# Optimization experiments

Hardware: AMD Instinct MI355X
Metric: run time of the kernel (lower is better)

The kernel has to match this reference:

```python
import jax, jax.numpy as jnp
import numpy as np

N_EMBD = 1024
HEAD_SIZE = 64


def setup_inputs() -> dict:
    key = jax.random.key(0)
    kx, kq, kk, kv = jax.random.split(key, 4)
    B, T = 8, 2048
    x = jax.random.normal(kx, (B, T, N_EMBD), dtype=jnp.float32)
    s = 1.0 / np.sqrt(N_EMBD)
    Wq = jax.random.normal(kq, (N_EMBD, HEAD_SIZE), dtype=jnp.float32) * s
    Wk = jax.random.normal(kk, (N_EMBD, HEAD_SIZE), dtype=jnp.float32) * s
    Wv = jax.random.normal(kv, (N_EMBD, HEAD_SIZE), dtype=jnp.float32) * s
    return {"x": x, "Wq": Wq, "Wk": Wk, "Wv": Wv}


def reference(x, Wq, Wk, Wv):
    # x: [B, T, C]; W*: [C, H]
    q = jnp.einsum('btc,ch->bth', x, Wq)
    k = jnp.einsum('btc,ch->bth', x, Wk)
    v = jnp.einsum('btc,ch->bth', x, Wv)
    H = q.shape[-1]
    score = jnp.einsum('bth,bsh->bts', q, k) / jnp.sqrt(jnp.asarray(H, q.dtype))
    T = score.shape[-1]
    causal = jnp.tril(jnp.ones((T, T), dtype=bool))  # [T, T]
    score = jnp.where(causal, score, -jnp.inf)
    attn = jax.nn.softmax(score, axis=-1)
    return jnp.einsum('bts,bsh->bth', attn, v)
```

## Files before the change

kernel.cpp:

```cpp
#include <hip/hip_runtime.h>

typedef __bf16 bf16;
typedef __attribute__((ext_vector_type(8))) __bf16 bf16x8;
typedef __attribute__((ext_vector_type(4))) __bf16 bf16x4;
typedef __attribute__((ext_vector_type(4))) float floatx4;

#define MFMA16(a, b, c) __builtin_amdgcn_mfma_f32_16x16x32_bf16((a), (b), (c), 0, 0, 0)

__global__ void prep_w(const float* __restrict__ Wq, const float* __restrict__ Wk,
                       const float* __restrict__ Wv, bf16* __restrict__ wTf) {
    int tid = blockIdx.x * 256 + threadIdx.x;
    int j = tid & 7;
    int l = (tid >> 3) & 15;
    int q = (tid >> 7) & 3;
    int kc = (tid >> 9) & 31;
    int mt = tid >> 14;
    int mat = mt >> 2;
    int h = ((mt & 3) << 4) + l;
    int c = kc * 32 + q * 8 + j;
    const float* W = (mat == 0) ? Wq : (mat == 1) ? Wk : Wv;
    wTf[tid] = (bf16)W[c * 64 + h];
}

#define XSTR 1032

__global__ __launch_bounds__(256, 4) void proj_qkv(const float* __restrict__ x,
                                                   const bf16* __restrict__ wTf,
                                                   bf16* __restrict__ q,
                                                   bf16* __restrict__ k,
                                                   bf16* __restrict__ vT) {
    __shared__ bf16 xs[16 * XSTR];

    const int tid = threadIdx.x;
    const int lane = tid & 63;
    const int w = tid >> 6;
    const int l15 = lane & 15;
    const int quad = lane >> 4;
    const int T0 = blockIdx.x * 16;

    {
        const int r = tid >> 4;
        const int cm = tid & 15;
        const float* g = x + (size_t)(T0 + r) * 1024 + cm * 8;
        floatx4 f[16];
        #pragma unroll
        for (int c = 0; c < 8; c++) {
            f[2 * c]     = *(const floatx4*)(g + c * 128);
            f[2 * c + 1] = *(const floatx4*)(g + c * 128 + 4);
        }
        bf16* ld = xs + r * XSTR + cm * 8;
        #pragma unroll
        for (int c = 0; c < 8; c++) {
            bf16x8 pk;
            pk[0] = (bf16)f[2*c][0]; pk[1] = (bf16)f[2*c][1];
            pk[2] = (bf16)f[2*c][2]; pk[3] = (bf16)f[2*c][3];
            pk[4] = (bf16)f[2*c+1][0]; pk[5] = (bf16)f[2*c+1][1];
            pk[6] = (bf16)f[2*c+1][2]; pk[7] = (bf16)f[2*c+1][3];
            *(bf16x8*)(ld + c * 128) = pk;
        }
    }
    __syncthreads();

    floatx4 acc[3] = {};
    const bf16* aw0 = wTf + (size_t)(w * 3 + 0) * 16384 + lane * 8;
    const bf16* aw1 = wTf + (size_t)(w * 3 + 1) * 16384 + lane * 8;
    const bf16* aw2 = wTf + (size_t)(w * 3 + 2) * 16384 + lane * 8;
    const bf16* xr = xs + l15 * XSTR + quad * 8;

    bf16x8 a0c = *(const bf16x8*)(aw0);
    bf16x8 a1c = *(const bf16x8*)(aw1);
    bf16x8 a2c = *(const bf16x8*)(aw2);
    bf16x8 a0n = *(const bf16x8*)(aw0 + 512);
    bf16x8 a1n = *(const bf16x8*)(aw1 + 512);
    bf16x8 a2n = *(const bf16x8*)(aw2 + 512);

    #pragma unroll 4
    for (int kc = 0; kc < 32; kc++) {
        bf16x8 p0 = *(const bf16x8*)(aw0 + (kc + 2) * 512);
        bf16x8 p1 = *(const bf16x8*)(aw1 + (kc + 2) * 512);
        bf16x8 p2 = *(const bf16x8*)(aw2 + (kc + 2) * 512);
        bf16x8 bb = *(const bf16x8*)(xr + kc * 32);
        acc[0] = MFMA16(a0c, bb, acc[0]);
        acc[1] = MFMA16(a1c, bb, acc[1]);
        acc[2] = MFMA16(a2c, bb, acc[2]);
        a0c = a0n; a1c = a1n; a2c = a2n;
        a0n = p0;  a1n = p1;  a2n = p2;
    }

    const int t = T0 + l15;
    #pragma unroll
    for (int i = 0; i < 3; i++) {
        int mtile = w * 3 + i;
        int mat = mtile >> 2;
        int hbase = ((mtile & 3) << 4) + (quad << 2);
        float sc = (mat == 0) ? 0.125f : 1.0f;
        bf16x4 pk;
        pk[0] = (bf16)(acc[i][0] * sc);
        pk[1] = (bf16)(acc[i][1] * sc);
        pk[2] = (bf16)(acc[i][2] * sc);
        pk[3] = (bf16)(acc[i][3] * sc);
        if (mat == 0) {
            *(bf16x4*)(q + (size_t)t * 64 + hbase) = pk;
        } else if (mat == 1) {
            *(bf16x4*)(k + (size_t)t * 64 + hbase) = pk;
        } else {
            int b = t >> 11, tt = t & 2047;
            #pragma unroll
            for (int r = 0; r < 4; r++)
                vT[(size_t)(b * 64 + hbase + r) * 2048 + tt] = pk[r];
        }
    }
}

#define KP2 72
#define OH 68

__global__ __launch_bounds__(512, 4) void flash(const bf16* __restrict__ q,
                                                const bf16* __restrict__ k,
                                                const bf16* __restrict__ vT,
                                                float* __restrict__ out) {
    __shared__ char smem[8 * 16 * OH * 4];
    __shared__ float Ms[8][16], Ls[8][16];
    bf16* psall = (bf16*)smem;
    float* Os = (float*)smem;

    const int b = blockIdx.x & 7;
    const int p = blockIdx.x >> 3;
    const int t0A = p * 16;
    const int t0B = (127 - p) * 16;
    const int nttA = (p >> 2) + 1;
    const int nttB = ((127 - p) >> 2) + 1;
    const int L = nttA + nttB;

    const int tid = threadIdx.x;
    const int w = tid >> 6;
    const int lane = tid & 63;
    const int l15 = lane & 15;
    const int quad = lane >> 4;

    const int s0 = (L * w) >> 3;
    const int s1 = (L * (w + 1)) >> 3;

    const bf16* kbase = k + (size_t)(b * 2048 + l15) * 64 + quad * 8;
    const bf16* vbase = vT + (size_t)(b * 64 + l15) * 2048 + quad * 8;
    bf16* psw = psall + w * 16 * KP2;

    const bf16* qpA = q + (size_t)(b * 2048 + t0A + l15) * 64 + quad * 8;
    const bf16* qpB = q + (size_t)(b * 2048 + t0B + l15) * 64 + quad * 8;

    floatx4 oA[4] = {}, oB[4] = {};
    float miA = -1e30f, liA = 0.f, miB = -1e30f, liB = 0.f;

#define KV_STEP(jtv, isdiag, t0v, qf0v, qf1v, mi_, li_, o_)                          \
    {                                                                                 \
        const bf16* kp = kbase + (size_t)(jtv) * 4096;                                \
        floatx4 stt[4];                                                               \
        _Pragma("unroll") for (int mt = 0; mt < 4; mt++) {                            \
            floatx4 z = {};                                                           \
            bf16x8 ka0 = *(const bf16x8*)(kp + mt * 1024);                            \
            bf16x8 ka1 = *(const bf16x8*)(kp + mt * 1024 + 32);                       \
            z = MFMA16(ka0, qf0v, z);                                                 \
            z = MFMA16(ka1, qf1v, z);                                                 \
            stt[mt] = z;                                                              \
        }                                                                             \
        if (isdiag) {                                                                 \
            _Pragma("unroll") for (int mt = 0; mt < 4; mt++)                          \
                _Pragma("unroll") for (int r = 0; r < 4; r++) {                       \
                    int kv = (jtv) * 64 + mt * 16 + quad * 4 + r;                     \
                    if (kv > (t0v) + l15) stt[mt][r] = -1e30f;                        \
                }                                                                     \
        }                                                                             \
        float mx = fmaxf(fmaxf(fmaxf(stt[0][0], stt[0][1]), fmaxf(stt[0][2], stt[0][3])),  \
                         fmaxf(fmaxf(stt[1][0], stt[1][1]), fmaxf(stt[1][2], stt[1][3]))); \
        mx = fmaxf(mx, fmaxf(fmaxf(fmaxf(stt[2][0], stt[2][1]), fmaxf(stt[2][2], stt[2][3])),  \
                             fmaxf(fmaxf(stt[3][0], stt[3][1]), fmaxf(stt[3][2], stt[3][3])))); \
        mx = fmaxf(mx, __shfl_xor(mx, 16, 64));                                       \
        mx = fmaxf(mx, __shfl_xor(mx, 32, 64));                                       \
        float mnew = fmaxf(mi_, mx);                                                  \
        float aa = __expf(mi_ - mnew);                                                \
        mi_ = mnew;                                                                   \
        float rs = 0.f;                                                               \
        _Pragma("unroll") for (int mt = 0; mt < 4; mt++)                              \
            _Pragma("unroll") for (int r = 0; r < 4; r++) {                           \
                float pv = __expf(stt[mt][r] - mnew);                                 \
                stt[mt][r] = pv;                                                      \
                rs += pv;                                                             \
            }                                                                         \
        rs += __shfl_xor(rs, 16, 64);                                                 \
        rs += __shfl_xor(rs, 32, 64);                                                 \
        li_ = li_ * aa + rs;                                                          \
        _Pragma("unroll") for (int mt = 0; mt < 4; mt++)                              \
            _Pragma("unroll") for (int r = 0; r < 4; r++) o_[mt][r] *= aa;            \
        _Pragma("unroll") for (int mt = 0; mt < 4; mt++) {                            \
            bf16x4 pk;                                                                \
            pk[0] = (bf16)stt[mt][0]; pk[1] = (bf16)stt[mt][1];                       \
            pk[2] = (bf16)stt[mt][2]; pk[3] = (bf16)stt[mt][3];                       \
            *(bf16x4*)(psw + l15 * KP2 + mt * 16 + quad * 4) = pk;                    \
        }                                                                             \
        const bf16* vp = vbase + (jtv) * 64;                                          \
        _Pragma("unroll") for (int kc = 0; kc < 2; kc++) {                            \
            bf16x8 pb = *(const bf16x8*)(psw + l15 * KP2 + kc * 32 + quad * 8);       \
            _Pragma("unroll") for (int mt = 0; mt < 4; mt++) {                        \
                bf16x8 va = *(const bf16x8*)(vp + mt * 32768 + kc * 32);              \
                o_[mt] = MFMA16(va, pb, o_[mt]);                                      \
            }                                                                         \
        }                                                                             \
    }

    {
        const int eA = (s1 < nttA) ? s1 : nttA;
        if (s0 < eA) {
            bf16x8 qf0 = *(const bf16x8*)qpA;
            bf16x8 qf1 = *(const bf16x8*)(qpA + 32);
            for (int s = s0; s < eA; s++) {
                KV_STEP(s, (s == nttA - 1), t0A, qf0, qf1, miA, liA, oA);
            }
        }
    }
    {
        const int sB = (s0 > nttA) ? s0 : nttA;
        if (sB < s1) {
            bf16x8 qf0 = *(const bf16x8*)qpB;
            bf16x8 qf1 = *(const bf16x8*)(qpB + 32);
            for (int s = sB; s < s1; s++) {
                KV_STEP(s - nttA, (s == L - 1), t0B, qf0, qf1, miB, liB, oB);
            }
        }
    }

    #pragma unroll
    for (int tile = 0; tile < 2; tile++) {
        __syncthreads();
        float mi = tile ? miB : miA;
        float li = tile ? liB : liA;
        if (lane < 16) { Ms[w][lane] = mi; Ls[w][lane] = li; }
        #pragma unroll
        for (int mt = 0; mt < 4; mt++) {
            floatx4 ov = tile ? oB[mt] : oA[mt];
            *(floatx4*)(Os + (w * 16 + l15) * OH + mt * 16 + quad * 4) = ov;
        }
        __syncthreads();
        {
            int qq = tid >> 5;
            int h2 = (tid & 31) * 2;
            float Mg = -1e30f;
            #pragma unroll
            for (int u = 0; u < 8; u++) Mg = fmaxf(Mg, Ms[u][qq]);
            float Lg = 0.f, v0 = 0.f, v1 = 0.f;
            #pragma unroll
            for (int u = 0; u < 8; u++) {
                float sw = __expf(Ms[u][qq] - Mg);
                Lg += sw * Ls[u][qq];
                const float* Or = Os + (u * 16 + qq) * OH + h2;
                v0 += sw * Or[0];
                v1 += sw * Or[1];
            }
            float inv = 1.0f / Lg;
            int t0v = tile ? t0B : t0A;
            float* op = out + (size_t)(b * 2048 + t0v + qq) * 64 + h2;
            op[0] = v0 * inv;
            op[1] = v1 * inv;
        }
    }
#undef KV_STEP
}

extern "C" void kernel_launch(void* const* d_in, const int* in_sizes, int n_in,
                              void* d_out, int out_size, void* d_ws, size_t ws_size,
                              hipStream_t stream) {
    const float* x  = (const float*)d_in[0];
    const float* Wq = (const float*)d_in[1];
    const float* Wk = (const float*)d_in[2];
    const float* Wv = (const float*)d_in[3];
    float* out = (float*)d_out;

    char* ws = (char*)d_ws;
    bf16* wTf = (bf16*)ws;
    bf16* q   = (bf16*)(ws + 397312);
    bf16* k   = (bf16*)(ws + 397312 + 2097152);
    bf16* vT  = (bf16*)(ws + 397312 + 2 * 2097152);

    hipLaunchKernelGGL(prep_w,   dim3(768),  dim3(256), 0, stream, Wq, Wk, Wv, wTf);
    hipLaunchKernelGGL(proj_qkv, dim3(1024), dim3(256), 0, stream, x, wTf, q, k, vT);
    hipLaunchKernelGGL(flash,    dim3(512),  dim3(512), 0, stream, q, k, vT, out);
}
```

Before: 144.1 us.

## Double projection row tile, swizzle LDS, and add lazy rescale with exp2 softmax

The projection kernel now handles 32 rows per block instead of 16, so each weight fragment loaded from global memory feeds two MFMAs. The x tile in shared memory uses an XOR swizzle in place of padding, and the grid is halved with launch bounds lowered to 2. In the flash kernel, Q is pre-scaled by log2(e)/8 so the softmax can use native exp2. The running-max rescale is skipped when the new max exceeds the old one by at most 8 (in log2 units), and s_setprio raises wave priority around the MFMA blocks. These changes cut weight-load traffic, exponential cost and rescale work, at the price of a larger LDS footprint per block, lower occupancy, and bounded growth of the unnormalized values.

Result: faster. 140.0 us (-2.9%).

```diff
diff --git a/kernel.cpp b/kernel.cpp
--- a/kernel.cpp
+++ b/kernel.cpp
@@ -22,50 +22,55 @@
     wTf[tid] = (bf16)W[c * 64 + h];
 }
 
-#define XSTR 1032
-
-__global__ __launch_bounds__(256, 4) void proj_qkv(const float* __restrict__ x,
+__global__ __launch_bounds__(256, 2) void proj_qkv(const float* __restrict__ x,
                                                    const bf16* __restrict__ wTf,
                                                    bf16* __restrict__ q,
                                                    bf16* __restrict__ k,
                                                    bf16* __restrict__ vT) {
-    __shared__ bf16 xs[16 * XSTR];
+    __shared__ __align__(16) char xsb[32 * 2048];
 
     const int tid = threadIdx.x;
     const int lane = tid & 63;
     const int w = tid >> 6;
     const int l15 = lane & 15;
     const int quad = lane >> 4;
-    const int T0 = blockIdx.x * 16;
+    const int T0 = blockIdx.x * 32;
 
     {
         const int r = tid >> 4;
         const int cm = tid & 15;
-        const float* g = x + (size_t)(T0 + r) * 1024 + cm * 8;
-        floatx4 f[16];
         #pragma unroll
-        for (int c = 0; c < 8; c++) {
-            f[2 * c]     = *(const floatx4*)(g + c * 128);
-            f[2 * c + 1] = *(const floatx4*)(g + c * 128 + 4);
-        }
-        bf16* ld = xs + r * XSTR + cm * 8;
-        #pragma unroll
-        for (int c = 0; c < 8; c++) {
-            bf16x8 pk;
-            pk[0] = (bf16)f[2*c][0]; pk[1] = (bf16)f[2*c][1];
-            pk[2] = (bf16)f[2*c][2]; pk[3] = (bf16)f[2*c][3];
-            pk[4] = (bf16)f[2*c+1][0]; pk[5] = (bf16)f[2*c+1][1];
-            pk[6] = (bf16)f[2*c+1][2]; pk[7] = (bf16)f[2*c+1][3];
-            *(bf16x8*)(ld + c * 128) = pk;
+        for (int half = 0; half < 2; half++) {
+            const int row = r + half * 16;
+            const float* g = x + (size_t)(T0 + row) * 1024 + cm * 8;
+            floatx4 f[16];
+            #pragma unroll
+            for (int c = 0; c < 8; c++) {
+                f[2 * c]     = *(const floatx4*)(g + c * 128);
+                f[2 * c + 1] = *(const floatx4*)(g + c * 128 + 4);
+            }
+            char* ldb = xsb + row * 2048;
+            const int sxs = (row & 7) << 4;
+            #pragma unroll
+            for (int c = 0; c < 8; c++) {
+                bf16x8 pk;
+                pk[0] = (bf16)f[2*c][0]; pk[1] = (bf16)f[2*c][1];
+                pk[2] = (bf16)f[2*c][2]; pk[3] = (bf16)f[2*c][3];
+                pk[4] = (bf16)f[2*c+1][0]; pk[5] = (bf16)f[2*c+1][1];
+                pk[6] = (bf16)f[2*c+1][2]; pk[7] = (bf16)f[2*c+1][3];
+                *(bf16x8*)(ldb + ((cm * 16 + c * 256) ^ sxs)) = pk;
+            }
         }
     }
     __syncthreads();
 
-    floatx4 acc[3] = {};
+    floatx4 acc[6] = {};
     const bf16* aw0 = wTf + (size_t)(w * 3 + 0) * 16384 + lane * 8;
     const bf16* aw1 = wTf + (size_t)(w * 3 + 1) * 16384 + lane * 8;
     const bf16* aw2 = wTf + (size_t)(w * 3 + 2) * 16384 + lane * 8;
-    const bf16* xr = xs + l15 * XSTR + quad * 8;
+    const char* xr = xsb + l15 * 2048;
+    const int sx = (l15 & 7) << 4;
+    const int q16 = quad * 16;
 
     bf16x8 a0c = *(const bf16x8*)(aw0);
     bf16x8 a1c = *(const bf16x8*)(aw1);
@@ -79,35 +84,44 @@
         bf16x8 p0 = *(const bf16x8*)(aw0 + (kc + 2) * 512);
         bf16x8 p1 = *(const bf16x8*)(aw1 + (kc + 2) * 512);
         bf16x8 p2 = *(const bf16x8*)(aw2 + (kc + 2) * 512);
-        bf16x8 bb = *(const bf16x8*)(xr + kc * 32);
-        acc[0] = MFMA16(a0c, bb, acc[0]);
-        acc[1] = MFMA16(a1c, bb, acc[1]);
-        acc[2] = MFMA16(a2c, bb, acc[2]);
+        const int o = (kc * 64 + q16) ^ sx;
+        bf16x8 b0 = *(const bf16x8*)(xr + o);
+        bf16x8 b1 = *(const bf16x8*)(xr + 32768 + o);
+        acc[0] = MFMA16(a0c, b0, acc[0]);
+        acc[1] = MFMA16(a0c, b1, acc[1]);
+        acc[2] = MFMA16(a1c, b0, acc[2]);
+        acc[3] = MFMA16(a1c, b1, acc[3]);
+        acc[4] = MFMA16(a2c, b0, acc[4]);
+        acc[5] = MFMA16(a2c, b1, acc[5]);
         a0c = a0n; a1c = a1n; a2c = a2n;
         a0n = p0;  a1n = p1;  a2n = p2;
     }
 
-    const int t = T0 + l15;
     #pragma unroll
     for (int i = 0; i < 3; i++) {
         int mtile = w * 3 + i;
         int mat = mtile >> 2;
         int hbase = ((mtile & 3) << 4) + (quad << 2);
-        float sc = (mat == 0) ? 0.125f : 1.0f;
-        bf16x4 pk;
-        pk[0] = (bf16)(acc[i][0] * sc);
-        pk[1] = (bf16)(acc[i][1] * sc);
-        pk[2] = (bf16)(acc[i][2] * sc);
-        pk[3] = (bf16)(acc[i][3] * sc);
-        if (mat == 0) {
-            *(bf16x4*)(q + (size_t)t * 64 + hbase) = pk;
-        } else if (mat == 1) {
-            *(bf16x4*)(k + (size_t)t * 64 + hbase) = pk;
-        } else {
-            int b = t >> 11, tt = t & 2047;
-            #pragma unroll
-            for (int r = 0; r < 4; r++)
-                vT[(size_t)(b * 64 + hbase + r) * 2048 + tt] = pk[r];
+        float sc = (mat == 0) ? 0.18033688011112042f : 1.0f;
+        #pragma unroll
+        for (int tt = 0; tt < 2; tt++) {
+            const int t = T0 + tt * 16 + l15;
+            floatx4 av = acc[i * 2 + tt];
+            bf16x4 pk;
+            pk[0] = (bf16)(av[0] * sc);
+            pk[1] = (bf16)(av[1] * sc);
+            pk[2] = (bf16)(av[2] * sc);
+            pk[3] = (bf16)(av[3] * sc);
+            if (mat == 0) {
+                *(bf16x4*)(q + (size_t)t * 64 + hbase) = pk;
+            } else if (mat == 1) {
+                *(bf16x4*)(k + (size_t)t * 64 + hbase) = pk;
+            } else {
+                int bidx = t >> 11, tmod = t & 2047;
+                #pragma unroll
+                for (int r = 0; r < 4; r++)
+                    vT[(size_t)(bidx * 64 + hbase + r) * 2048 + tmod] = pk[r];
+            }
         }
     }
 }
@@ -155,6 +169,7 @@
     {                                                                                 \
         const bf16* kp = kbase + (size_t)(jtv) * 4096;                                \
         floatx4 stt[4];                                                               \
+        __builtin_amdgcn_s_setprio(1);                                                \
         _Pragma("unroll") for (int mt = 0; mt < 4; mt++) {                            \
             floatx4 z = {};                                                           \
             bf16x8 ka0 = *(const bf16x8*)(kp + mt * 1024);                            \
@@ -163,6 +178,7 @@
             z = MFMA16(ka1, qf1v, z);                                                 \
             stt[mt] = z;                                                              \
         }                                                                             \
+        __builtin_amdgcn_s_setprio(0);                                                \
         if (isdiag) {                                                                 \
             _Pragma("unroll") for (int mt = 0; mt < 4; mt++)                          \
                 _Pragma("unroll") for (int r = 0; r < 4; r++) {                       \
@@ -176,21 +192,25 @@
                              fmaxf(fmaxf(stt[3][0], stt[3][1]), fmaxf(stt[3][2], stt[3][3])))); \
         mx = fmaxf(mx, __shfl_xor(mx, 16, 64));                                       \
         mx = fmaxf(mx, __shfl_xor(mx, 32, 64));                                       \
-        float mnew = fmaxf(mi_, mx);                                                  \
-        float aa = __expf(mi_ - mnew);                                                \
-        mi_ = mnew;                                                                   \
+        const bool nodefer = !__all(mx - mi_ <= 8.0f);                                \
+        const float mnew = nodefer ? fmaxf(mi_, mx) : mi_;                            \
         float rs = 0.f;                                                               \
         _Pragma("unroll") for (int mt = 0; mt < 4; mt++)                              \
             _Pragma("unroll") for (int r = 0; r < 4; r++) {                           \
-                float pv = __expf(stt[mt][r] - mnew);                                 \
+                float pv = __builtin_amdgcn_exp2f(stt[mt][r] - mnew);                 \
                 stt[mt][r] = pv;                                                      \
                 rs += pv;                                                             \
             }                                                                         \
         rs += __shfl_xor(rs, 16, 64);                                                 \
         rs += __shfl_xor(rs, 32, 64);                                                 \
-        li_ = li_ * aa + rs;                                                          \
-        _Pragma("unroll") for (int mt = 0; mt < 4; mt++)                              \
-            _Pragma("unroll") for (int r = 0; r < 4; r++) o_[mt][r] *= aa;            \
+        if (nodefer) {                                                                \
+            const float aa = __builtin_amdgcn_exp2f(mi_ - mnew);                      \
+            mi_ = mnew;                                                               \
+            li_ *= aa;                                                                \
+            _Pragma("unroll") for (int mt = 0; mt < 4; mt++)                          \
+                _Pragma("unroll") for (int r = 0; r < 4; r++) o_[mt][r] *= aa;        \
+        }                                                                             \
+        li_ += rs;                                                                    \
         _Pragma("unroll") for (int mt = 0; mt < 4; mt++) {                            \
             bf16x4 pk;                                                                \
             pk[0] = (bf16)stt[mt][0]; pk[1] = (bf16)stt[mt][1];                       \
@@ -198,6 +218,7 @@
             *(bf16x4*)(psw + l15 * KP2 + mt * 16 + quad * 4) = pk;                    \
         }                                                                             \
         const bf16* vp = vbase + (jtv) * 64;                                          \
+        __builtin_amdgcn_s_setprio(1);                                                \
         _Pragma("unroll") for (int kc = 0; kc < 2; kc++) {                            \
             bf16x8 pb = *(const bf16x8*)(psw + l15 * KP2 + kc * 32 + quad * 8);       \
             _Pragma("unroll") for (int mt = 0; mt < 4; mt++) {                        \
@@ -205,6 +226,7 @@
                 o_[mt] = MFMA16(va, pb, o_[mt]);                                      \
             }                                                                         \
         }                                                                             \
+        __builtin_amdgcn_s_setprio(0);                                                \
     }
 
     {
@@ -249,7 +271,7 @@
             float Lg = 0.f, v0 = 0.f, v1 = 0.f;
             #pragma unroll
             for (int u = 0; u < 8; u++) {
-                float sw = __expf(Ms[u][qq] - Mg);
+                float sw = __builtin_amdgcn_exp2f(Ms[u][qq] - Mg);
                 Lg += sw * Ls[u][qq];
                 const float* Or = Os + (u * 16 + qq) * OH + h2;
                 v0 += sw * Or[0];
@@ -280,7 +302,7 @@
     bf16* k   = (bf16*)(ws + 397312 + 2097152);
     bf16* vT  = (bf16*)(ws + 397312 + 2 * 2097152);
 
-    hipLaunchKernelGGL(prep_w,   dim3(768),  dim3(256), 0, stream, Wq, Wk, Wv, wTf);
-    hipLaunchKernelGGL(proj_qkv, dim3(1024), dim3(256), 0, stream, x, wTf, q, k, vT);
-    hipLaunchKernelGGL(flash,    dim3(512),  dim3(512), 0, stream, q, k, vT, out);
+    hipLaunchKernelGGL(prep_w,   dim3(768), dim3(256), 0, stream, Wq, Wk, Wv, wTf);
+    hipLaunchKernelGGL(proj_qkv, dim3(512), dim3(256), 0, stream, x, wTf, q, k, vT);
+    hipLaunchKernelGGL(flash,    dim3(512), dim3(512), 0, stream, q, k, vT, out);
 }
```
